# Performance work log

Hardware: AMD Instinct MI355X
Metric: run time of the kernel (lower is better)

The kernel has to match this reference:

```python
import jax, jax.numpy as jnp
import numpy as np

B, N, D_IN, D_OUT = 2, 2048, 2048, 2048
H, G = 32, 8            # num_heads, num_kv_groups
HD = D_OUT // H         # head_dim = 64
R = H // G              # group_size = 4


def _rope(x, cos, sin):
    # x: (b, h, n, hd); cos/sin: (n, hd)
    hd = x.shape[-1]
    x1, x2 = x[..., : hd // 2], x[..., hd // 2:]
    rotated = jnp.concatenate((-x2, x1), axis=-1)
    return x * cos[None, None] + rotated * sin[None, None]


def setup_inputs() -> dict:
    key = jax.random.key(0)
    ks = jax.random.split(key, 6)
    x = jax.random.normal(ks[0], (B, N, D_IN), dtype=jnp.float32)
    # standard RoPE tables over full head_dim (rotate-half convention)
    inv_freq = 1.0 / (10000.0 ** (np.arange(0, HD, 2, dtype=np.float32) / HD))
    t = np.arange(N, dtype=np.float32)
    freqs = np.outer(t, inv_freq)                      # (n, hd/2)
    emb = np.concatenate([freqs, freqs], axis=-1)      # (n, hd)
    cos = jnp.asarray(np.cos(emb), dtype=jnp.float32)
    sin = jnp.asarray(np.sin(emb), dtype=jnp.float32)
    mask = jnp.triu(jnp.ones((N, N), dtype=bool), k=1)  # True above diagonal -> masked
    s = 0.02
    Wq = jax.random.normal(ks[1], (D_IN, D_OUT), dtype=jnp.float32) * s
    Wk = jax.random.normal(ks[2], (D_IN, G * HD), dtype=jnp.float32) * s
    Wv = jax.random.normal(ks[3], (D_IN, G * HD), dtype=jnp.float32) * s
    Wo = jax.random.normal(ks[4], (D_OUT, D_OUT), dtype=jnp.float32) * s
    return {"x": x, "cos": cos, "sin": sin, "mask": mask,
            "Wq": Wq, "Wk": Wk, "Wv": Wv, "Wo": Wo}


def reference(x, cos, sin, mask, Wq, Wk, Wv, Wo):
    b, n, _ = x.shape
    q = (x @ Wq).reshape(b, n, H, HD).transpose(0, 2, 1, 3)   # (b, H, n, hd)
    k = (x @ Wk).reshape(b, n, G, HD).transpose(0, 2, 1, 3)   # (b, G, n, hd)
    v = (x @ Wv).reshape(b, n, G, HD).transpose(0, 2, 1, 3)   # (b, G, n, hd)
    q = _rope(q, cos, sin)
    k = _rope(k, cos, sin)
    # grouped attention: avoid physically repeating KV heads
    qg = q.reshape(b, G, R, n, HD)                            # (b, G, r, n, hd)
    scores = jnp.einsum('bgrnd,bgmd->bgrnm', qg, k)           # (b, G, r, n, n)
    scores = jnp.where(mask[None, None, None], -jnp.inf, scores)
    attn = jax.nn.softmax(scores / jnp.sqrt(jnp.float32(HD)), axis=-1)
    ctx = jnp.einsum('bgrnm,bgmd->bgrnd', attn, v)            # (b, G, r, n, hd)
    ctx = ctx.reshape(b, H, n, HD).transpose(0, 2, 1, 3).reshape(b, n, D_OUT)
    return ctx @ Wo
```

## Files before the change

### kernel.cpp

```cpp
#include <hip/hip_runtime.h>
#include <hip/hip_bf16.h>
#include <stdint.h>

#define B_   2
#define N_   2048
#define DIN  2048
#define DOUT 2048
#define H_   32
#define G_   8
#define HD_  64
#define M_   (B_*N_)

using short8 = __attribute__((ext_vector_type(8))) short;
using f32x4  = __attribute__((ext_vector_type(4))) float;
using f32x16 = __attribute__((ext_vector_type(16))) float;
using int4v  = __attribute__((ext_vector_type(4))) int;

__device__ __forceinline__ unsigned short f2bf(float f) {
  unsigned int u = __float_as_uint(f);
  unsigned int r = u + 0x7FFFu + ((u >> 16) & 1u);
  return (unsigned short)(r >> 16);
}
__device__ __forceinline__ float bf2f(unsigned short h) {
  return __uint_as_float(((unsigned int)h) << 16);
}

__global__ void k_cvt(const float* __restrict__ in, unsigned short* __restrict__ out, int n4) {
  int i = blockIdx.x * 256 + threadIdx.x;
  if (i >= n4) return;
  float4 v = reinterpret_cast<const float4*>(in)[i];
  uint2 o;
  o.x = (unsigned int)f2bf(v.x) | ((unsigned int)f2bf(v.y) << 16);
  o.y = (unsigned int)f2bf(v.z) | ((unsigned int)f2bf(v.w) << 16);
  reinterpret_cast<uint2*>(out)[i] = o;
}

__global__ void k_transpose_all(const float* __restrict__ Wq, const float* __restrict__ Wk,
                                const float* __restrict__ Wv, const float* __restrict__ Wo,
                                unsigned short* __restrict__ Wqkv_t,
                                unsigned short* __restrict__ Wo_t) {
  __shared__ float tile[32][33];
  const int ct = blockIdx.x;
  const int r0 = blockIdx.y * 32;
  const float* W;
  unsigned short* dst;
  int C, c0, dstRow;
  if (ct < 64)      { W = Wq; dst = Wqkv_t; C = 2048; c0 = ct*32;      dstRow = c0; }
  else if (ct < 80) { W = Wk; dst = Wqkv_t; C = 512;  c0 = (ct-64)*32; dstRow = 2048 + c0; }
  else if (ct < 96) { W = Wv; dst = Wqkv_t; C = 512;  c0 = (ct-80)*32; dstRow = 2560 + c0; }
  else              { W = Wo; dst = Wo_t;   C = 2048; c0 = (ct-96)*32; dstRow = c0; }
  const int tx = threadIdx.x, ty = threadIdx.y;
  #pragma unroll
  for (int j = 0; j < 4; ++j)
    tile[ty + j*8][tx] = W[(size_t)(r0 + ty + j*8) * C + c0 + tx];
  __syncthreads();
  #pragma unroll
  for (int j = 0; j < 4; ++j)
    dst[(size_t)(dstRow + ty + j*8) * 2048 + r0 + tx] = f2bf(tile[tx][ty + j*8]);
}

#define A0OFF 0
#define B0OFF 32768
#define A1OFF 65536
#define B1OFF 98304

#define QPHASE(ABUF, M0, STAGES, WAITS)                                          \
  {                                                                              \
    short8 a00 = rdA(ABUF, M0, 0),   a01 = rdA(ABUF, M0, 1);                     \
    short8 a10 = rdA(ABUF, M0+1, 0), a11 = rdA(ABUF, M0+1, 1);                   \
    STAGES;                                                                      \
    WAITS;                                                                       \
    __builtin_amdgcn_s_barrier();                                                \
    asm volatile("s_waitcnt lgkmcnt(0)" ::: "memory");                           \
    __builtin_amdgcn_sched_barrier(0);                                           \
    __builtin_amdgcn_s_setprio(1);                                               \
    _Pragma("unroll")                                                            \
    for (int n = 0; n < 4; ++n) {                                                \
      acc[M0][n]   = __builtin_amdgcn_mfma_f32_16x16x32_bf16(a00, bv[n][0], acc[M0][n], 0,0,0);   \
      acc[M0][n]   = __builtin_amdgcn_mfma_f32_16x16x32_bf16(a01, bv[n][1], acc[M0][n], 0,0,0);   \
      acc[M0+1][n] = __builtin_amdgcn_mfma_f32_16x16x32_bf16(a10, bv[n][0], acc[M0+1][n], 0,0,0); \
      acc[M0+1][n] = __builtin_amdgcn_mfma_f32_16x16x32_bf16(a11, bv[n][1], acc[M0+1][n], 0,0,0); \
    }                                                                            \
    __builtin_amdgcn_s_setprio(0);                                               \
    __builtin_amdgcn_s_barrier();                                                \
  }

__global__ void __launch_bounds__(512, 2)
k_gemm_qkv(const unsigned short* __restrict__ A, const unsigned short* __restrict__ Bt,
           unsigned short* __restrict__ Qp, unsigned short* __restrict__ Kp,
           unsigned short* __restrict__ Vp,
           const float* __restrict__ cosT, const float* __restrict__ sinT) {
  __shared__ unsigned short sm[65536];
  const int tid = threadIdx.x;
  const int wid = tid >> 6, l = tid & 63;
  const int lrow = l & 15, lk = l >> 4;
  const int wm = wid >> 2, wn = wid & 3;

  const int gx   = gridDim.x;
  const int nwg  = gx * gridDim.y;
  const int orig = blockIdx.y * gx + blockIdx.x;
  const int q8   = nwg >> 3;
  const int xcd  = orig & 7, lin = orig >> 3;
  const int wg   = xcd * q8 + lin;
  const int bx   = wg % gx, by = wg / gx;
  const int rowA0 = by * 256, rowB0 = bx * 256;

  f32x4 acc[8][4];
  #pragma unroll
  for (int m = 0; m < 8; ++m)
    #pragma unroll
    for (int n = 0; n < 4; ++n)
      #pragma unroll
      for (int r = 0; r < 4; ++r) acc[m][n][r] = 0.f;

  const int srowoff = wid*8 + (l >> 3);
  const int skoff   = (((l & 7) ^ ((l >> 3) & 7)) << 3);
  auto stageHalf = [&](const unsigned short* Mat, int rowBase, int t, int bufByte, int half) {
    #pragma unroll
    for (int j = 0; j < 2; ++j) {
      const unsigned short* g = Mat + (size_t)(rowBase + half*128 + j*64 + srowoff) * 2048
                                    + t*64 + skoff;
      __builtin_amdgcn_global_load_lds(
          (const __attribute__((address_space(1))) unsigned int*)g,
          (__attribute__((address_space(3))) unsigned int*)
              ((char*)sm + bufByte + half*16384 + j*8192 + wid*1024),
          16, 0, 0);
    }
  };

  const int aswz = (lrow & 7) << 4;
  auto rdA = [&](int bufByte, int m, int kk) -> short8 {
    int byte = bufByte + (wm*128 + m*16 + lrow)*128 + ((kk*64 + lk*16) ^ aswz);
    return *reinterpret_cast<const short8*>((char*)sm + byte);
  };
  auto rdB = [&](int bufByte, int n, int kk) -> short8 {
    int byte = bufByte + (wn*64 + n*16 + lrow)*128 + ((kk*64 + lk*16) ^ aswz);
    return *reinterpret_cast<const short8*>((char*)sm + byte);
  };

  short8 bv[4][2];

  stageHalf(Bt, rowB0, 0, B0OFF, 0); stageHalf(Bt, rowB0, 0, B0OFF, 1);
  stageHalf(A,  rowA0, 0, A0OFF, 0); stageHalf(A,  rowA0, 0, A0OFF, 1);
  stageHalf(Bt, rowB0, 1, B1OFF, 0); stageHalf(Bt, rowB0, 1, B1OFF, 1);
  asm volatile("s_waitcnt vmcnt(4)" ::: "memory");
  __builtin_amdgcn_sched_barrier(0);
  __builtin_amdgcn_s_barrier();

  for (int i = 0; i < 16; ++i) {
    const int t = 2*i;
    const bool more = (i < 15);

    #pragma unroll
    for (int n = 0; n < 4; ++n) { bv[n][0] = rdB(B0OFF, n, 0); bv[n][1] = rdB(B0OFF, n, 1); }
    QPHASE(A0OFF, 0, { stageHalf(A, rowA0, t+1, A1OFF, 0);
                       stageHalf(A, rowA0, t+1, A1OFF, 1); }, {});
    QPHASE(A0OFF, 2, { if (more) stageHalf(Bt, rowB0, t+2, B0OFF, 0); }, {});
    QPHASE(A0OFF, 4, { if (more) stageHalf(Bt, rowB0, t+2, B0OFF, 1); }, {});
    QPHASE(A0OFF, 6, {}, { if (more) { asm volatile("s_waitcnt vmcnt(4)" ::: "memory"); }
                           else      { asm volatile("s_waitcnt vmcnt(0)" ::: "memory"); }
                           __builtin_amdgcn_sched_barrier(0); });

    #pragma unroll
    for (int n = 0; n < 4; ++n) { bv[n][0] = rdB(B1OFF, n, 0); bv[n][1] = rdB(B1OFF, n, 1); }
    QPHASE(A1OFF, 0, { if (more) stageHalf(A, rowA0, t+2, A0OFF, 0); }, {});
    QPHASE(A1OFF, 2, { if (more) stageHalf(A, rowA0, t+2, A0OFF, 1); }, {});
    QPHASE(A1OFF, 4, { if (more) stageHalf(Bt, rowB0, t+3, B1OFF, 0); }, {});
    QPHASE(A1OFF, 6, { if (more) { stageHalf(Bt, rowB0, t+3, B1OFF, 1);
                                   asm volatile("s_waitcnt vmcnt(4)" ::: "memory");
                                   __builtin_amdgcn_sched_barrier(0); } }, {});
  }

  if (rowB0 >= 2560) {
    const int bq = rowA0 >> 11;
    #pragma unroll
    for (int m = 0; m < 8; ++m) {
      const int row0 = rowA0 + wm*128 + m*16 + lk*4;
      const int key  = row0 & 2047;
      const size_t tbase = (size_t)(key >> 5)*2048 + (size_t)((key >> 4) & 1)*512
                         + (size_t)((key >> 3) & 1)*256 + (size_t)(key & 7);
      #pragma unroll
      for (int n = 0; n < 4; ++n) {
        const int cv = rowB0 + wn*64 + n*16 + lrow - 2560;
        const int gq = cv >> 6, d = cv & 63;
        const size_t addr = (size_t)(bq*8 + gq)*131072 + tbase
                          + (size_t)(d >> 5)*1024 + (size_t)(d & 31)*8;
        ushort4 st;
        st.x = f2bf(acc[m][n][0]); st.y = f2bf(acc[m][n][1]);
        st.z = f2bf(acc[m][n][2]); st.w = f2bf(acc[m][n][3]);
        *reinterpret_cast<ushort4*>(Vp + addr) = st;
      }
    }
  } else {
    const bool isQ = (rowB0 < 2048);
    const float scale = isQ ? 0.18033688011112042f : 1.0f;
    unsigned short* dst = isQ ? Qp : Kp;
    #pragma unroll
    for (int m = 0; m < 8; ++m) {
      const int row0 = rowA0 + wm*128 + m*16 + lk*4;
      const int b = row0 >> 11;
      #pragma unroll
      for (int n = 0; n < 2; ++n) {
        const int col = rowB0 + wn*64 + n*16 + lrow;
        const int e   = n*16 + lrow;
        const int hg  = isQ ? (col >> 6) : ((col - 2048) >> 6);
        const size_t chunk = (size_t)(isQ ? (b*32 + hg) : (b*8 + hg)) * 64;
        #pragma unroll
        for (int r = 0; r < 4; ++r) {
          const int pos = (row0 + r) & 2047;
          const float cc = cosT[pos*64 + e] * scale;
          const float ss = sinT[pos*64 + e] * scale;
          const float x1 = acc[m][n][r];
          const float x2 = acc[m][n+2][r];
          const size_t off = (chunk + (pos >> 5)) * 2048
                           + (size_t)(e >> 4)*512 + (size_t)((e >> 3) & 1)*256
                           + (size_t)(pos & 31)*8 + (e & 7);
          dst[off]        = f2bf(x1*cc - x2*ss);
          dst[off + 1024] = f2bf(x2*cc + x1*ss);
        }
      }
    }
  }
}

__global__ void __launch_bounds__(256, 3)
k_gemm_out(const unsigned short* __restrict__ A, const unsigned short* __restrict__ Bt,
           float* __restrict__ C) {
  __shared__ unsigned short As[128 * 32];
  __shared__ unsigned short Bs[128 * 32];
  const int K = DOUT, N = DOUT;
  const int tid  = threadIdx.x;
  const int wid  = tid >> 6, l = tid & 63;
  const int lrow = l & 15,  lk = l >> 4;
  const int wm = wid >> 1,  wn = wid & 1;

  const int gx   = gridDim.x;
  const int nwg  = gx * gridDim.y;
  const int orig = blockIdx.y * gx + blockIdx.x;
  const int q8   = nwg >> 3;
  const int xcd  = orig & 7, lin = orig >> 3;
  const int wg   = xcd * q8 + lin;
  const int bx   = wg % gx, by = wg / gx;

  const int rowA0 = by * 128, rowB0 = bx * 128;

  f32x4 acc[4][4];
  #pragma unroll
  for (int m = 0; m < 4; ++m)
    #pragma unroll
    for (int n = 0; n < 4; ++n)
      #pragma unroll
      for (int r = 0; r < 4; ++r) acc[m][n][r] = 0.f;

  int srow[2], scol[2];
  #pragma unroll
  for (int issue = 0; issue < 2; ++issue) {
    int slot = issue*4096 + wid*1024 + l*16;
    int row  = slot >> 6;
    int cp   = (slot >> 4) & 3;
    int sw   = (row & 3) ^ ((row >> 2) & 3);
    srow[issue] = row;
    scol[issue] = (cp ^ sw) * 8;
  }
  const int swr    = (lrow & 3) ^ ((lrow >> 2) & 3);
  const int rchunk = (lk ^ swr) * 8;

  for (int kt = 0; kt < K; kt += 32) {
    __syncthreads();
    #pragma unroll
    for (int issue = 0; issue < 2; ++issue) {
      const unsigned short* ga = A  + (size_t)(rowA0 + srow[issue]) * K + kt + scol[issue];
      const unsigned short* gb = Bt + (size_t)(rowB0 + srow[issue]) * K + kt + scol[issue];
      __builtin_amdgcn_global_load_lds(
          (const __attribute__((address_space(1))) unsigned int*)ga,
          (__attribute__((address_space(3))) unsigned int*)((char*)As + issue*4096 + wid*1024),
          16, 0, 0);
      __builtin_amdgcn_global_load_lds(
          (const __attribute__((address_space(1))) unsigned int*)gb,
          (__attribute__((address_space(3))) unsigned int*)((char*)Bs + issue*4096 + wid*1024),
          16, 0, 0);
    }
    asm volatile("s_waitcnt vmcnt(0)" ::: "memory");
    __syncthreads();

    short8 av[4], bvv[4];
    #pragma unroll
    for (int m = 0; m < 4; ++m)
      av[m] = *reinterpret_cast<const short8*>(&As[(wm*64 + m*16 + lrow)*32 + rchunk]);
    #pragma unroll
    for (int n = 0; n < 4; ++n)
      bvv[n] = *reinterpret_cast<const short8*>(&Bs[(wn*64 + n*16 + lrow)*32 + rchunk]);
    #pragma unroll
    for (int m = 0; m < 4; ++m)
      #pragma unroll
      for (int n = 0; n < 4; ++n)
        acc[m][n] = __builtin_amdgcn_mfma_f32_16x16x32_bf16(av[m], bvv[n], acc[m][n], 0, 0, 0);
  }

  #pragma unroll
  for (int m = 0; m < 4; ++m) {
    int row0 = rowA0 + wm*64 + m*16 + lk*4;
    #pragma unroll
    for (int n = 0; n < 4; ++n) {
      int col = rowB0 + wn*64 + n*16 + lrow;
      #pragma unroll
      for (int r = 0; r < 4; ++r)
        C[(size_t)(row0 + r) * N + col] = acc[m][n][r];
    }
  }
}

__global__ void __launch_bounds__(256, 3)
k_attn(const unsigned short* __restrict__ Qp, const unsigned short* __restrict__ Kp,
       const unsigned short* __restrict__ Vp, unsigned short* __restrict__ ctx) {
  __shared__ unsigned short kvlds[2][4096];
  const int bid = blockIdx.x;
  const int c   = bid & 15;
  const int b   = c >> 3, g = c & 7;
  const int w   = bid >> 4;
  const int jj  = w >> 4, x = w & 15;
  const int qt  = (jj == 0) ? 63 - x : (jj == 1) ? 32 + x : (jj == 2) ? 31 - x : x;
  const int tid = threadIdx.x;
  const int hh  = tid >> 6;
  const int h   = g*4 + hh;
  const int l   = tid & 63;
  const int lq  = l & 31, hi = l >> 5;

  const unsigned short* qbase = Qp + ((size_t)(b*32 + h)*64 + qt)*2048 + l*8;
  short8 qf0 = *reinterpret_cast<const short8*>(qbase);
  short8 qf1 = *reinterpret_cast<const short8*>(qbase + 512);
  short8 qf2 = *reinterpret_cast<const short8*>(qbase + 1024);
  short8 qf3 = *reinterpret_cast<const short8*>(qbase + 1536);

  const unsigned short* ksrc = Kp + (size_t)c*131072 + hh*512 + l*8;
  const unsigned short* vsrc = Vp + (size_t)c*131072 + hh*512 + l*8;

  f32x16 acc0, acc1;
  #pragma unroll
  for (int r = 0; r < 16; ++r) { acc0[r] = 0.f; acc1[r] = 0.f; }
  float l_run = 0.f;

  auto stage = [&](int t, int buf) {
    __builtin_amdgcn_global_load_lds(
        (const __attribute__((address_space(1))) unsigned int*)(ksrc + (size_t)t*2048),
        (__attribute__((address_space(3))) unsigned int*)((char*)&kvlds[buf][0] + hh*1024),
        16, 0, 0);
    __builtin_amdgcn_global_load_lds(
        (const __attribute__((address_space(1))) unsigned int*)(vsrc + (size_t)t*2048),
        (__attribute__((address_space(3))) unsigned int*)((char*)&kvlds[buf][2048] + hh*1024),
        16, 0, 0);
  };

  auto body = [&](bool diag, int buf) {
    short8 ka = *reinterpret_cast<const short8*>(&kvlds[buf][l*8]);
    short8 kb = *reinterpret_cast<const short8*>(&kvlds[buf][512 + l*8]);
    short8 kc = *reinterpret_cast<const short8*>(&kvlds[buf][1024 + l*8]);
    short8 kd = *reinterpret_cast<const short8*>(&kvlds[buf][1536 + l*8]);

    f32x16 s;
    #pragma unroll
    for (int r = 0; r < 16; ++r) s[r] = 0.f;
    __builtin_amdgcn_s_setprio(1);
    s = __builtin_amdgcn_mfma_f32_32x32x16_bf16(ka, qf0, s, 0, 0, 0);
    s = __builtin_amdgcn_mfma_f32_32x32x16_bf16(kb, qf1, s, 0, 0, 0);
    s = __builtin_amdgcn_mfma_f32_32x32x16_bf16(kc, qf2, s, 0, 0, 0);
    s = __builtin_amdgcn_mfma_f32_32x32x16_bf16(kd, qf3, s, 0, 0, 0);
    __builtin_amdgcn_s_setprio(0);

    if (diag) {
      #pragma unroll
      for (int r = 0; r < 16; ++r) {
        const int ko = (r & 3) + 8*(r >> 2) + 4*hi;
        s[r] = (ko <= lq) ? s[r] : -3.0e38f;
      }
    }

    unsigned int w8[8];
    float ps = 0.f;
    #pragma unroll
    for (int i = 0; i < 8; ++i) {
      float p0 = exp2f(s[2*i]);
      float p1 = exp2f(s[2*i+1]);
      ps += p0 + p1;
      asm("v_cvt_pk_bf16_f32 %0, %1, %2" : "=v"(w8[i]) : "v"(p0), "v"(p1));
    }
    ps += __shfl_xor(ps, 32);
    l_run += ps;

    unsigned int x0 = w8[0], x1 = w8[1], y0 = w8[2], y1 = w8[3];
    asm("v_permlane32_swap_b32 %0, %1" : "+v"(x0), "+v"(y0));
    asm("v_permlane32_swap_b32 %0, %1" : "+v"(x1), "+v"(y1));
    unsigned int x2 = w8[4], x3 = w8[5], y2 = w8[6], y3 = w8[7];
    asm("v_permlane32_swap_b32 %0, %1" : "+v"(x2), "+v"(y2));
    asm("v_permlane32_swap_b32 %0, %1" : "+v"(x3), "+v"(y3));
    int4v p0i, p1i;
    p0i[0] = (int)x0; p0i[1] = (int)x1; p0i[2] = (int)y0; p0i[3] = (int)y1;
    p1i[0] = (int)x2; p1i[1] = (int)x3; p1i[2] = (int)y2; p1i[3] = (int)y3;
    short8 pa0 = __builtin_bit_cast(short8, p0i);
    short8 pa1 = __builtin_bit_cast(short8, p1i);

    short8 va = *reinterpret_cast<const short8*>(&kvlds[buf][2048 + l*8]);
    short8 vb = *reinterpret_cast<const short8*>(&kvlds[buf][2560 + l*8]);
    short8 vc = *reinterpret_cast<const short8*>(&kvlds[buf][3072 + l*8]);
    short8 vd = *reinterpret_cast<const short8*>(&kvlds[buf][3584 + l*8]);

    __builtin_amdgcn_s_setprio(1);
    acc0 = __builtin_amdgcn_mfma_f32_32x32x16_bf16(va, pa0, acc0, 0, 0, 0);
    acc0 = __builtin_amdgcn_mfma_f32_32x32x16_bf16(vb, pa1, acc0, 0, 0, 0);
    acc1 = __builtin_amdgcn_mfma_f32_32x32x16_bf16(vc, pa0, acc1, 0, 0, 0);
    acc1 = __builtin_amdgcn_mfma_f32_32x32x16_bf16(vd, pa1, acc1, 0, 0, 0);
    __builtin_amdgcn_s_setprio(0);
  };

  stage(0, 0);
  __syncthreads();
  for (int t = 0; ; ) {
    const int cur = t & 1;
    if (t < qt) stage(t + 1, cur ^ 1);
    body(t == qt, cur);
    if (++t > qt) break;
    __syncthreads();
  }

  const float rl = 1.f / l_run;
  unsigned short* op = ctx + (size_t)(b*N_ + qt*32 + lq) * DOUT + h*HD_ + 4*hi;
  #pragma unroll
  for (int dt = 0; dt < 2; ++dt) {
    #pragma unroll
    for (int rq = 0; rq < 4; ++rq) {
      const float a0 = (dt ? acc1[4*rq+0] : acc0[4*rq+0]) * rl;
      const float a1 = (dt ? acc1[4*rq+1] : acc0[4*rq+1]) * rl;
      const float a2 = (dt ? acc1[4*rq+2] : acc0[4*rq+2]) * rl;
      const float a3 = (dt ? acc1[4*rq+3] : acc0[4*rq+3]) * rl;
      ushort4 st;
      st.x = f2bf(a0); st.y = f2bf(a1); st.z = f2bf(a2); st.w = f2bf(a3);
      *reinterpret_cast<ushort4*>(op + dt*32 + rq*8) = st;
    }
  }
}

extern "C" void kernel_launch(void* const* d_in, const int* in_sizes, int n_in,
                              void* d_out, int out_size, void* d_ws, size_t ws_size,
                              hipStream_t stream) {
  const float* x    = (const float*)d_in[0];
  const float* cosT = (const float*)d_in[1];
  const float* sinT = (const float*)d_in[2];
  const float* Wq   = (const float*)d_in[4];
  const float* Wk   = (const float*)d_in[5];
  const float* Wv   = (const float*)d_in[6];
  const float* Wo   = (const float*)d_in[7];
  float* out = (float*)d_out;

  char* ws = (char*)d_ws;
  unsigned short* xb     = (unsigned short*)(ws);
  unsigned short* ctxb   = xb;
  unsigned short* Wqkv_t = (unsigned short*)(ws + 16777216);
  unsigned short* Wo_t   = (unsigned short*)(ws + 29360128);
  unsigned short* Qp     = (unsigned short*)(ws + 37748736);
  unsigned short* Kp     = (unsigned short*)(ws + 54525952);
  unsigned short* Vp     = (unsigned short*)(ws + 58720256);

  k_cvt<<<dim3(M_*DIN/4/256), dim3(256), 0, stream>>>(x, xb, M_*DIN/4);

  k_transpose_all<<<dim3(160, 64), dim3(32, 8), 0, stream>>>(
      Wq, Wk, Wv, Wo, Wqkv_t, Wo_t);

  k_gemm_qkv<<<dim3(3072/256, M_/256), 512, 0, stream>>>(
      xb, Wqkv_t, Qp, Kp, Vp, cosT, sinT);

  k_attn<<<dim3(1024), dim3(256), 0, stream>>>(Qp, Kp, Vp, ctxb);

  k_gemm_out<<<dim3(DOUT/128, M_/128), 256, 0, stream>>>(ctxb, Wo_t, out);
}
```

Baseline: 183.5 us.

## Rewrite output projection GEMM with 256x128 tiles and double-buffered LDS pipeline

The output-projection GEMM moves to 512-thread blocks computing 256x128 tiles with a 64-wide K step. A and B tiles are double-buffered in LDS through async global-to-LDS loads, and those loads are interleaved with MFMA phases using explicit barriers and priority hints. An XOR swizzle is applied to the LDS layout. The goal is to hide global load latency and remove the per-iteration full sync and vmcnt(0) stall of the old single-buffered loop, at the cost of more LDS per block and lower occupancy.

```diff
diff --git a/kernel.cpp b/kernel.cpp
--- a/kernel.cpp
+++ b/kernel.cpp
@@ -223,16 +223,37 @@
   }
 }
 
-__global__ void __launch_bounds__(256, 3)
+#define OA0 0
+#define OB0 32768
+#define OA1 49152
+#define OB1 81920
+
+#define OPHASE(ABUF, M, STAGES, WAITS)                                           \
+  {                                                                              \
+    short8 a0 = rdA(ABUF, M, 0), a1 = rdA(ABUF, M, 1);                           \
+    STAGES;                                                                      \
+    WAITS;                                                                       \
+    __builtin_amdgcn_s_barrier();                                                \
+    asm volatile("s_waitcnt lgkmcnt(0)" ::: "memory");                           \
+    __builtin_amdgcn_sched_barrier(0);                                           \
+    __builtin_amdgcn_s_setprio(1);                                               \
+    _Pragma("unroll")                                                            \
+    for (int n = 0; n < 4; ++n) {                                                \
+      acc[M][n] = __builtin_amdgcn_mfma_f32_16x16x32_bf16(a0, bv[n][0], acc[M][n], 0,0,0); \
+      acc[M][n] = __builtin_amdgcn_mfma_f32_16x16x32_bf16(a1, bv[n][1], acc[M][n], 0,0,0); \
+    }                                                                            \
+    __builtin_amdgcn_s_setprio(0);                                               \
+    __builtin_amdgcn_s_barrier();                                                \
+  }
+
+__global__ void __launch_bounds__(512, 2)
 k_gemm_out(const unsigned short* __restrict__ A, const unsigned short* __restrict__ Bt,
            float* __restrict__ C) {
-  __shared__ unsigned short As[128 * 32];
-  __shared__ unsigned short Bs[128 * 32];
-  const int K = DOUT, N = DOUT;
-  const int tid  = threadIdx.x;
-  const int wid  = tid >> 6, l = tid & 63;
-  const int lrow = l & 15,  lk = l >> 4;
-  const int wm = wid >> 1,  wn = wid & 1;
+  __shared__ unsigned short sm[49152];
+  const int tid = threadIdx.x;
+  const int wid = tid >> 6, l = tid & 63;
+  const int lrow = l & 15, lk = l >> 4;
+  const int wm = wid >> 1, wn = wid & 1;
 
   const int gx   = gridDim.x;
   const int nwg  = gx * gridDim.y;
@@ -241,8 +262,7 @@
   const int xcd  = orig & 7, lin = orig >> 3;
   const int wg   = xcd * q8 + lin;
   const int bx   = wg % gx, by = wg / gx;
-
-  const int rowA0 = by * 128, rowB0 = bx * 128;
+  const int rowA0 = by * 256, rowB0 = bx * 128;
 
   f32x4 acc[4][4];
   #pragma unroll
@@ -252,49 +272,62 @@
       #pragma unroll
       for (int r = 0; r < 4; ++r) acc[m][n][r] = 0.f;
 
-  int srow[2], scol[2];
-  #pragma unroll
-  for (int issue = 0; issue < 2; ++issue) {
-    int slot = issue*4096 + wid*1024 + l*16;
-    int row  = slot >> 6;
-    int cp   = (slot >> 4) & 3;
-    int sw   = (row & 3) ^ ((row >> 2) & 3);
-    srow[issue] = row;
-    scol[issue] = (cp ^ sw) * 8;
-  }
-  const int swr    = (lrow & 3) ^ ((lrow >> 2) & 3);
-  const int rchunk = (lk ^ swr) * 8;
-
-  for (int kt = 0; kt < K; kt += 32) {
-    __syncthreads();
-    #pragma unroll
-    for (int issue = 0; issue < 2; ++issue) {
-      const unsigned short* ga = A  + (size_t)(rowA0 + srow[issue]) * K + kt + scol[issue];
-      const unsigned short* gb = Bt + (size_t)(rowB0 + srow[issue]) * K + kt + scol[issue];
-      __builtin_amdgcn_global_load_lds(
-          (const __attribute__((address_space(1))) unsigned int*)ga,
-          (__attribute__((address_space(3))) unsigned int*)((char*)As + issue*4096 + wid*1024),
-          16, 0, 0);
-      __builtin_amdgcn_global_load_lds(
-          (const __attribute__((address_space(1))) unsigned int*)gb,
-          (__attribute__((address_space(3))) unsigned int*)((char*)Bs + issue*4096 + wid*1024),
-          16, 0, 0);
-    }
-    asm volatile("s_waitcnt vmcnt(0)" ::: "memory");
-    __syncthreads();
-
-    short8 av[4], bvv[4];
-    #pragma unroll
-    for (int m = 0; m < 4; ++m)
-      av[m] = *reinterpret_cast<const short8*>(&As[(wm*64 + m*16 + lrow)*32 + rchunk]);
-    #pragma unroll
-    for (int n = 0; n < 4; ++n)
-      bvv[n] = *reinterpret_cast<const short8*>(&Bs[(wn*64 + n*16 + lrow)*32 + rchunk]);
-    #pragma unroll
-    for (int m = 0; m < 4; ++m)
-      #pragma unroll
-      for (int n = 0; n < 4; ++n)
-        acc[m][n] = __builtin_amdgcn_mfma_f32_16x16x32_bf16(av[m], bvv[n], acc[m][n], 0, 0, 0);
+  const int srowoff = wid*8 + (l >> 3);
+  const int skoff   = (((l & 7) ^ ((l >> 3) & 7)) << 3);
+  auto stageU = [&](const unsigned short* Mat, int rowBase, int t, int bufByte, int u) {
+    const unsigned short* g = Mat + (size_t)(rowBase + u*64 + srowoff) * 2048 + t*64 + skoff;
+    __builtin_amdgcn_global_load_lds(
+        (const __attribute__((address_space(1))) unsigned int*)g,
+        (__attribute__((address_space(3))) unsigned int*)
+            ((char*)sm + bufByte + u*8192 + wid*1024),
+        16, 0, 0);
+  };
+
+  const int aswz = (lrow & 7) << 4;
+  auto rdA = [&](int bufByte, int m, int kk) -> short8 {
+    int byte = bufByte + (wm*64 + m*16 + lrow)*128 + ((kk*64 + lk*16) ^ aswz);
+    return *reinterpret_cast<const short8*>((char*)sm + byte);
+  };
+  auto rdB = [&](int bufByte, int n, int kk) -> short8 {
+    int byte = bufByte + (wn*64 + n*16 + lrow)*128 + ((kk*64 + lk*16) ^ aswz);
+    return *reinterpret_cast<const short8*>((char*)sm + byte);
+  };
+
+  short8 bv[4][2];
+
+  stageU(Bt, rowB0, 0, OB0, 0); stageU(Bt, rowB0, 0, OB0, 1);
+  stageU(A,  rowA0, 0, OA0, 0); stageU(A,  rowA0, 0, OA0, 1);
+  stageU(A,  rowA0, 0, OA0, 2); stageU(A,  rowA0, 0, OA0, 3);
+  stageU(Bt, rowB0, 1, OB1, 0); stageU(Bt, rowB0, 1, OB1, 1);
+  asm volatile("s_waitcnt vmcnt(2)" ::: "memory");
+  __builtin_amdgcn_sched_barrier(0);
+  __builtin_amdgcn_s_barrier();
+
+  for (int i = 0; i < 16; ++i) {
+    const int t = 2*i;
+    const bool more = (i < 15);
+
+    #pragma unroll
+    for (int n = 0; n < 4; ++n) { bv[n][0] = rdB(OB0, n, 0); bv[n][1] = rdB(OB0, n, 1); }
+    OPHASE(OA0, 0, { stageU(A, rowA0, t+1, OA1, 0); stageU(A, rowA0, t+1, OA1, 1); }, {});
+    OPHASE(OA0, 1, { stageU(A, rowA0, t+1, OA1, 2); stageU(A, rowA0, t+1, OA1, 3); }, {});
+    OPHASE(OA0, 2, { if (more) { stageU(Bt, rowB0, t+2, OB0, 0);
+                                 stageU(Bt, rowB0, t+2, OB0, 1); } }, {});
+    OPHASE(OA0, 3, {}, { if (more) { asm volatile("s_waitcnt vmcnt(2)" ::: "memory"); }
+                         else      { asm volatile("s_waitcnt vmcnt(0)" ::: "memory"); }
+                         __builtin_amdgcn_sched_barrier(0); });
+
+    #pragma unroll
+    for (int n = 0; n < 4; ++n) { bv[n][0] = rdB(OB1, n, 0); bv[n][1] = rdB(OB1, n, 1); }
+    OPHASE(OA1, 0, { if (more) { stageU(A, rowA0, t+2, OA0, 0);
+                                 stageU(A, rowA0, t+2, OA0, 1); } }, {});
+    OPHASE(OA1, 1, { if (more) { stageU(A, rowA0, t+2, OA0, 2);
+                                 stageU(A, rowA0, t+2, OA0, 3); } }, {});
+    OPHASE(OA1, 2, { if (more) { stageU(Bt, rowB0, t+3, OB1, 0);
+                                 stageU(Bt, rowB0, t+3, OB1, 1); } }, {});
+    OPHASE(OA1, 3, {}, { if (more) { asm volatile("s_waitcnt vmcnt(2)" ::: "memory"); }
+                         else      { asm volatile("s_waitcnt vmcnt(0)" ::: "memory"); }
+                         __builtin_amdgcn_sched_barrier(0); });
   }
 
   #pragma unroll
@@ -305,7 +338,7 @@
       int col = rowB0 + wn*64 + n*16 + lrow;
       #pragma unroll
       for (int r = 0; r < 4; ++r)
-        C[(size_t)(row0 + r) * N + col] = acc[m][n][r];
+        C[(size_t)(row0 + r) * DOUT + col] = acc[m][n][r];
     }
   }
 }
@@ -470,5 +503,5 @@
 
   k_attn<<<dim3(1024), dim3(256), 0, stream>>>(Qp, Kp, Vp, ctxb);
 
-  k_gemm_out<<<dim3(DOUT/128, M_/128), 256, 0, stream>>>(ctxb, Wo_t, out);
-}
+  k_gemm_out<<<dim3(DOUT/128, M_/256), 512, 0, stream>>>(ctxb, Wo_t, out);
+}
```

Result: faster. 173.5 us (-5.5%).
